# Kernel optimization log

Measured on AMD Instinct MI355X. Metric: run time of the kernel, lower is better.

## Reference

```python
import jax, jax.numpy as jnp
import numpy as np

MASK_RATIO = 0.02
N2V_W, WAV_W, TV_W = 1.0, 0.2, 0.01
THRESHOLD = 50.0
LEVELS = 3


def setup_inputs() -> dict:
    key = jax.random.key(0)
    k1, k2, k3 = jax.random.split(key, 3)
    shape = (64, 1, 512, 512)
    pred = jax.random.uniform(k1, shape, dtype=jnp.float32)
    noisy_input = jax.random.uniform(k2, shape, dtype=jnp.float32)
    # N2V random blind-spot mask (torch.rand_like(pred) < mask_ratio)
    mask = jax.random.uniform(k3, shape, dtype=jnp.float32) < MASK_RATIO
    return {"pred": pred, "noisy_input": noisy_input, "mask": mask}


def haar_dwt2(x):
    # x: [B, H, W] with H, W even. Single-level 2D Haar DWT (pywt 'haar').
    a = x[:, 0::2, 0::2]
    b = x[:, 0::2, 1::2]
    c = x[:, 1::2, 0::2]
    d = x[:, 1::2, 1::2]
    ll = (a + b + c + d) * 0.5
    ch = (a + b - c - d) * 0.5  # horizontal detail
    cv = (a - b + c - d) * 0.5  # vertical detail
    cd = (a - b - c + d) * 0.5  # diagonal detail
    return ll, ch, cv, cd


def _level_l1(c, thr):
    # L1 between coeff and its (detached) soft-thresholded version
    target = jax.lax.stop_gradient(jnp.sign(c) * jnp.maximum(jnp.abs(c) - thr, 0.0))
    return jnp.mean(jnp.abs(c - target))


def reference(pred, noisy_input, mask):
    p = jnp.clip(pred, 0.0, 1.0)

    # --- Noise2Void masked L1 ---
    m = mask.astype(p.dtype)
    n2v = jnp.sum(jnp.abs(p - noisy_input) * m) / jnp.maximum(jnp.sum(m), 1.0)

    # --- Wavelet sparsity (multi-level Haar, soft-threshold targets) ---
    x = p[:, 0]  # [B, H, W]
    details = []  # finest first
    for _ in range(LEVELS):
        x, ch, cv, cd = haar_dwt2(x)
        details.append((ch, cv, cd))
    wav = jnp.asarray(0.0, dtype=p.dtype)
    for level_idx in range(1, LEVELS + 1):  # level_idx=1 -> coarsest (wavedec2 order)
        ch, cv, cd = details[LEVELS - level_idx]
        thr = (THRESHOLD / (2.0 ** (level_idx - 1))) / 255.0
        lvl = (_level_l1(ch, thr) + _level_l1(cv, thr) + _level_l1(cd, thr)) / 3.0
        wav = wav + (1.0 / level_idx) * lvl

    # --- Total variation ---
    tv = jnp.mean(jnp.abs(p[:, :, 1:, :] - p[:, :, :-1, :])) + \
         jnp.mean(jnp.abs(p[:, :, :, 1:] - p[:, :, :, :-1]))

    return N2V_W * n2v + WAV_W * wav + TV_W * tv
```

## Files before the change

### kernel.cpp

```cpp
#include <hip/hip_runtime.h>

#define NIMG 64
#define H 512
#define W 512

constexpr float THR_64  = 50.0f / 255.0f;
constexpr float THR_128 = 50.0f / 2.0f / 255.0f;
constexpr float THR_256 = 50.0f / 4.0f / 255.0f;

__device__ __forceinline__ float wave_sum(float v) {
#pragma unroll
    for (int o = 32; o > 0; o >>= 1) v += __shfl_down(v, o, 64);
    return v;
}

__device__ __forceinline__ float clip01(float x) {
    return fminf(fmaxf(x, 0.0f), 1.0f);
}

__device__ __forceinline__ float4 clip4(float4 p) {
    p.x = clip01(p.x); p.y = clip01(p.y); p.z = clip01(p.z); p.w = clip01(p.w);
    return p;
}

__global__ __launch_bounds__(256, 4) void kA(const float* __restrict__ pred,
                                             const float* __restrict__ noisy,
                                             const int* __restrict__ mask,
                                             float4* __restrict__ pA,
                                             float* __restrict__ pW2,
                                             float* __restrict__ ll2) {
    __shared__ float red[4][5];

    const int tid = threadIdx.x;
    const int lane = tid & 63;
    const int wv = tid >> 6;
    const int w = (blockIdx.x << 2) + wv;
    const int n = w >> 8;
    const int rem = w & 255;
    const int q = rem >> 1;
    const int h = rem & 1;
    const int r0 = q << 2;
    const int col = (h << 8) + (lane << 2);
    const size_t base = (size_t)n * (H * W) + (size_t)r0 * W + col;
    const bool has_halo = (q > 0);
    const size_t baseH = has_halo ? (base - W) : base;

    float4 p0 = *reinterpret_cast<const float4*>(pred + base);
    float4 p1 = *reinterpret_cast<const float4*>(pred + base + W);
    float4 p2 = *reinterpret_cast<const float4*>(pred + base + 2 * W);
    float4 p3 = *reinterpret_cast<const float4*>(pred + base + 3 * W);
    float4 hl = *reinterpret_cast<const float4*>(pred + baseH);
    float4 nz0 = *reinterpret_cast<const float4*>(noisy + base);
    float4 nz1 = *reinterpret_cast<const float4*>(noisy + base + W);
    float4 nz2 = *reinterpret_cast<const float4*>(noisy + base + 2 * W);
    float4 nz3 = *reinterpret_cast<const float4*>(noisy + base + 3 * W);
    int4 mk0 = *reinterpret_cast<const int4*>(mask + base);
    int4 mk1 = *reinterpret_cast<const int4*>(mask + base + W);
    int4 mk2 = *reinterpret_cast<const int4*>(mask + base + 2 * W);
    int4 mk3 = *reinterpret_cast<const int4*>(mask + base + 3 * W);
    float e0 = 0.f, e1 = 0.f, e2 = 0.f, e3 = 0.f;
    const bool edge = (h == 0) && (lane == 63);
    if (edge) {
        e0 = clip01(pred[base + 4]);
        e1 = clip01(pred[base + W + 4]);
        e2 = clip01(pred[base + 2 * W + 4]);
        e3 = clip01(pred[base + 3 * W + 4]);
    }

    p0 = clip4(p0); p1 = clip4(p1); p2 = clip4(p2); p3 = clip4(p3);
    hl = clip4(hl);

    float n2v = 0.0f, msum = 0.0f;
    {
        float m;
        m = mk0.x ? 1.f : 0.f; n2v += fabsf(p0.x - nz0.x) * m; msum += m;
        m = mk0.y ? 1.f : 0.f; n2v += fabsf(p0.y - nz0.y) * m; msum += m;
        m = mk0.z ? 1.f : 0.f; n2v += fabsf(p0.z - nz0.z) * m; msum += m;
        m = mk0.w ? 1.f : 0.f; n2v += fabsf(p0.w - nz0.w) * m; msum += m;
        m = mk1.x ? 1.f : 0.f; n2v += fabsf(p1.x - nz1.x) * m; msum += m;
        m = mk1.y ? 1.f : 0.f; n2v += fabsf(p1.y - nz1.y) * m; msum += m;
        m = mk1.z ? 1.f : 0.f; n2v += fabsf(p1.z - nz1.z) * m; msum += m;
        m = mk1.w ? 1.f : 0.f; n2v += fabsf(p1.w - nz1.w) * m; msum += m;
        m = mk2.x ? 1.f : 0.f; n2v += fabsf(p2.x - nz2.x) * m; msum += m;
        m = mk2.y ? 1.f : 0.f; n2v += fabsf(p2.y - nz2.y) * m; msum += m;
        m = mk2.z ? 1.f : 0.f; n2v += fabsf(p2.z - nz2.z) * m; msum += m;
        m = mk2.w ? 1.f : 0.f; n2v += fabsf(p2.w - nz2.w) * m; msum += m;
        m = mk3.x ? 1.f : 0.f; n2v += fabsf(p3.x - nz3.x) * m; msum += m;
        m = mk3.y ? 1.f : 0.f; n2v += fabsf(p3.y - nz3.y) * m; msum += m;
        m = mk3.z ? 1.f : 0.f; n2v += fabsf(p3.z - nz3.z) * m; msum += m;
        m = mk3.w ? 1.f : 0.f; n2v += fabsf(p3.w - nz3.w) * m; msum += m;
    }

    float tv = 0.0f;
    tv += fabsf(p0.y - p0.x) + fabsf(p0.z - p0.y) + fabsf(p0.w - p0.z);
    tv += fabsf(p1.y - p1.x) + fabsf(p1.z - p1.y) + fabsf(p1.w - p1.z);
    tv += fabsf(p2.y - p2.x) + fabsf(p2.z - p2.y) + fabsf(p2.w - p2.z);
    tv += fabsf(p3.y - p3.x) + fabsf(p3.z - p3.y) + fabsf(p3.w - p3.z);
    float nx0 = __shfl_down(p0.x, 1, 64);
    float nx1 = __shfl_down(p1.x, 1, 64);
    float nx2 = __shfl_down(p2.x, 1, 64);
    float nx3 = __shfl_down(p3.x, 1, 64);
    if (lane < 63) {
        tv += fabsf(nx0 - p0.w) + fabsf(nx1 - p1.w)
            + fabsf(nx2 - p2.w) + fabsf(nx3 - p3.w);
    }
    if (edge) {
        tv += fabsf(e0 - p0.w) + fabsf(e1 - p1.w)
            + fabsf(e2 - p2.w) + fabsf(e3 - p3.w);
    }
    tv += fabsf(p1.x - p0.x) + fabsf(p1.y - p0.y) + fabsf(p1.z - p0.z) + fabsf(p1.w - p0.w);
    tv += fabsf(p2.x - p1.x) + fabsf(p2.y - p1.y) + fabsf(p2.z - p1.z) + fabsf(p2.w - p1.w);
    tv += fabsf(p3.x - p2.x) + fabsf(p3.y - p2.y) + fabsf(p3.z - p2.z) + fabsf(p3.w - p2.w);
    if (has_halo) {
        tv += fabsf(p0.x - hl.x) + fabsf(p0.y - hl.y)
            + fabsf(p0.z - hl.z) + fabsf(p0.w - hl.w);
    }

    float wav1 = 0.0f;
    float llA0, llA1, llB0, llB1;
    {
        float a, b, c, d, ch, cv, cd;
        a = p0.x; b = p0.y; c = p1.x; d = p1.y;
        llA0 = (a + b + c + d) * 0.5f;
        ch = (a + b - c - d) * 0.5f; cv = (a - b + c - d) * 0.5f; cd = (a - b - c + d) * 0.5f;
        wav1 += fminf(fabsf(ch), THR_256) + fminf(fabsf(cv), THR_256) + fminf(fabsf(cd), THR_256);
        a = p0.z; b = p0.w; c = p1.z; d = p1.w;
        llA1 = (a + b + c + d) * 0.5f;
        ch = (a + b - c - d) * 0.5f; cv = (a - b + c - d) * 0.5f; cd = (a - b - c + d) * 0.5f;
        wav1 += fminf(fabsf(ch), THR_256) + fminf(fabsf(cv), THR_256) + fminf(fabsf(cd), THR_256);
        a = p2.x; b = p2.y; c = p3.x; d = p3.y;
        llB0 = (a + b + c + d) * 0.5f;
        ch = (a + b - c - d) * 0.5f; cv = (a - b + c - d) * 0.5f; cd = (a - b - c + d) * 0.5f;
        wav1 += fminf(fabsf(ch), THR_256) + fminf(fabsf(cv), THR_256) + fminf(fabsf(cd), THR_256);
        a = p2.z; b = p2.w; c = p3.z; d = p3.w;
        llB1 = (a + b + c + d) * 0.5f;
        ch = (a + b - c - d) * 0.5f; cv = (a - b + c - d) * 0.5f; cd = (a - b - c + d) * 0.5f;
        wav1 += fminf(fabsf(ch), THR_256) + fminf(fabsf(cv), THR_256) + fminf(fabsf(cd), THR_256);
    }

    float wav2;
    {
        float a = llA0, b = llA1, c = llB0, d = llB1;
        float ll2v = (a + b + c + d) * 0.5f;
        float ch = (a + b - c - d) * 0.5f;
        float cv = (a - b + c - d) * 0.5f;
        float cd = (a - b - c + d) * 0.5f;
        wav2 = fminf(fabsf(ch), THR_128) + fminf(fabsf(cv), THR_128) + fminf(fabsf(cd), THR_128);
        ll2[(size_t)n * 16384 + (size_t)q * 128 + (h << 6) + lane] = ll2v;
    }

    float v0 = wave_sum(n2v);
    float v1 = wave_sum(msum);
    float v2 = wave_sum(tv);
    float v3 = wave_sum(wav1);
    float v4 = wave_sum(wav2);
    if (lane == 0) {
        red[wv][0] = v0; red[wv][1] = v1; red[wv][2] = v2;
        red[wv][3] = v3; red[wv][4] = v4;
    }
    __syncthreads();
    if (tid == 0) {
        pA[blockIdx.x] = make_float4(red[0][0] + red[1][0] + red[2][0] + red[3][0],
                                     red[0][1] + red[1][1] + red[2][1] + red[3][1],
                                     red[0][2] + red[1][2] + red[2][2] + red[3][2],
                                     red[0][3] + red[1][3] + red[2][3] + red[3][3]);
        pW2[blockIdx.x] = red[0][4] + red[1][4] + red[2][4] + red[3][4];
    }
}

__global__ __launch_bounds__(256) void kC(const float* __restrict__ ll2,
                                          float* __restrict__ pC) {
    __shared__ float red[4];
    const int tid = threadIdx.x;
    const int lane = tid & 63, wv = tid >> 6;
    const int bid = blockIdx.x;
    const int n = bid >> 1;
    const int s = bid & 1;
    const float* src = ll2 + (size_t)n * 16384;

    float wav3 = 0.0f;
#pragma unroll
    for (int i = 0; i < 8; ++i) {
        int u = (i << 8) + tid;
        int qr = (s << 5) + (u >> 6);
        int qc = u & 63;
        float2 top = *reinterpret_cast<const float2*>(src + (2 * qr) * 128 + 2 * qc);
        float2 bot = *reinterpret_cast<const float2*>(src + (2 * qr + 1) * 128 + 2 * qc);
        float a = top.x, b = top.y, c = bot.x, d = bot.y;
        float ch = (a + b - c - d) * 0.5f;
        float cv = (a - b + c - d) * 0.5f;
        float cd = (a - b - c + d) * 0.5f;
        wav3 += fminf(fabsf(ch), THR_64) + fminf(fabsf(cv), THR_64) + fminf(fabsf(cd), THR_64);
    }
    float v = wave_sum(wav3);
    if (lane == 0) red[wv] = v;
    __syncthreads();
    if (tid == 0) pC[bid] = red[0] + red[1] + red[2] + red[3];
}

__global__ __launch_bounds__(256) void kD(const float4* __restrict__ pA,
                                          const float* __restrict__ pW2,
                                          const float* __restrict__ pC,
                                          float* __restrict__ out) {
    __shared__ float red[4][6];
    const int tid = threadIdx.x;
    const int lane = tid & 63, wv = tid >> 6;

    float s0 = 0, s1 = 0, s2 = 0, s3 = 0, s4 = 0, s5 = 0;
#pragma unroll
    for (int j = 0; j < 16; ++j) {
        float4 v = pA[tid + (j << 8)];
        s0 += v.x; s1 += v.y; s2 += v.z; s3 += v.w;
        s4 += pW2[tid + (j << 8)];
    }
    if (tid < 128) s5 = pC[tid];

    s0 = wave_sum(s0); s1 = wave_sum(s1); s2 = wave_sum(s2);
    s3 = wave_sum(s3); s4 = wave_sum(s4); s5 = wave_sum(s5);
    if (lane == 0) {
        red[wv][0] = s0; red[wv][1] = s1; red[wv][2] = s2;
        red[wv][3] = s3; red[wv][4] = s4; red[wv][5] = s5;
    }
    __syncthreads();
    if (tid == 0) {
        float a0 = red[0][0] + red[1][0] + red[2][0] + red[3][0];
        float a1 = red[0][1] + red[1][1] + red[2][1] + red[3][1];
        float a2 = red[0][2] + red[1][2] + red[2][2] + red[3][2];
        float a3 = red[0][3] + red[1][3] + red[2][3] + red[3][3];
        float a4 = red[0][4] + red[1][4] + red[2][4] + red[3][4];
        float a5 = red[0][5] + red[1][5] + red[2][5] + red[3][5];
        float n2v = a0 / fmaxf(a1, 1.0f);
        float tv = a2 / 16744448.0f;
        float wav = a3 * (1.0f / 37748736.0f)
                  + a4 * (1.0f / 6291456.0f)
                  + a5 * (1.0f / 786432.0f);
        out[0] = 1.0f * n2v + 0.2f * wav + 0.01f * tv;
    }
}

extern "C" void kernel_launch(void* const* d_in, const int* in_sizes, int n_in,
                              void* d_out, int out_size, void* d_ws, size_t ws_size,
                              hipStream_t stream) {
    (void)in_sizes; (void)n_in; (void)out_size; (void)ws_size;
    const float* pred  = (const float*)d_in[0];
    const float* noisy = (const float*)d_in[1];
    const int*   mask  = (const int*)d_in[2];

    float4* pA  = (float4*)d_ws;
    float*  pW2 = (float*)((char*)d_ws + 65536);
    float*  pC  = (float*)((char*)d_ws + 81920);
    float*  ll2 = (float*)((char*)d_ws + 98304);

    kA<<<4096, 256, 0, stream>>>(pred, noisy, mask, pA, pW2, ll2);
    kC<<<128, 256, 0, stream>>>(ll2, pC);
    kD<<<1, 256, 0, stream>>>(pA, pW2, pC, (float*)d_out);
}
```

Before: 197.5 us.

## Stage 8-row pred tiles in LDS with one halo row per block

Each block now loads a contiguous 8-row by 512-column tile of pred, noisy and mask with fully coalesced float4 loads, clips pred once and writes it to shared memory, plus a single halo row. The per-wave TV and Haar computations then read from LDS, so the redundant halo-row and edge-column global loads are replaced by shared reads. It adds a __syncthreads and 18 KB of LDS per block, and drops the occupancy hint from launch bounds. The grid mapping changes from 4 waves of independent 4-row strips to 64 blocks per image.

```diff
diff --git a/kernel.cpp b/kernel.cpp
--- a/kernel.cpp
+++ b/kernel.cpp
@@ -23,73 +23,61 @@
     return p;
 }
 
-__global__ __launch_bounds__(256, 4) void kA(const float* __restrict__ pred,
-                                             const float* __restrict__ noisy,
-                                             const int* __restrict__ mask,
-                                             float4* __restrict__ pA,
-                                             float* __restrict__ pW2,
-                                             float* __restrict__ ll2) {
+__global__ __launch_bounds__(256) void kA(const float* __restrict__ pred,
+                                          const float* __restrict__ noisy,
+                                          const int* __restrict__ mask,
+                                          float4* __restrict__ pA,
+                                          float* __restrict__ pW2,
+                                          float* __restrict__ ll2) {
+    __shared__ float sl[9 * 512];
     __shared__ float red[4][5];
 
     const int tid = threadIdx.x;
     const int lane = tid & 63;
     const int wv = tid >> 6;
-    const int w = (blockIdx.x << 2) + wv;
-    const int n = w >> 8;
-    const int rem = w & 255;
-    const int q = rem >> 1;
-    const int h = rem & 1;
-    const int r0 = q << 2;
-    const int col = (h << 8) + (lane << 2);
-    const size_t base = (size_t)n * (H * W) + (size_t)r0 * W + col;
-    const bool has_halo = (q > 0);
-    const size_t baseH = has_halo ? (base - W) : base;
-
-    float4 p0 = *reinterpret_cast<const float4*>(pred + base);
-    float4 p1 = *reinterpret_cast<const float4*>(pred + base + W);
-    float4 p2 = *reinterpret_cast<const float4*>(pred + base + 2 * W);
-    float4 p3 = *reinterpret_cast<const float4*>(pred + base + 3 * W);
-    float4 hl = *reinterpret_cast<const float4*>(pred + baseH);
-    float4 nz0 = *reinterpret_cast<const float4*>(noisy + base);
-    float4 nz1 = *reinterpret_cast<const float4*>(noisy + base + W);
-    float4 nz2 = *reinterpret_cast<const float4*>(noisy + base + 2 * W);
-    float4 nz3 = *reinterpret_cast<const float4*>(noisy + base + 3 * W);
-    int4 mk0 = *reinterpret_cast<const int4*>(mask + base);
-    int4 mk1 = *reinterpret_cast<const int4*>(mask + base + W);
-    int4 mk2 = *reinterpret_cast<const int4*>(mask + base + 2 * W);
-    int4 mk3 = *reinterpret_cast<const int4*>(mask + base + 3 * W);
-    float e0 = 0.f, e1 = 0.f, e2 = 0.f, e3 = 0.f;
-    const bool edge = (h == 0) && (lane == 63);
-    if (edge) {
-        e0 = clip01(pred[base + 4]);
-        e1 = clip01(pred[base + W + 4]);
-        e2 = clip01(pred[base + 2 * W + 4]);
-        e3 = clip01(pred[base + 3 * W + 4]);
-    }
-
-    p0 = clip4(p0); p1 = clip4(p1); p2 = clip4(p2); p3 = clip4(p3);
-    hl = clip4(hl);
+    const int bid = blockIdx.x;
+    const int n = bid >> 6;
+    const int s = bid & 63;
+    const int r0 = s << 3;
+    const size_t base = (size_t)n * (H * W) + (size_t)r0 * W;
 
     float n2v = 0.0f, msum = 0.0f;
-    {
+#pragma unroll
+    for (int k = 0; k < 4; ++k) {
+        const int idx = tid + (k << 8);
+        const size_t off = base + (size_t)idx * 4;
+        float4 p = *reinterpret_cast<const float4*>(pred + off);
+        float4 nz = *reinterpret_cast<const float4*>(noisy + off);
+        int4 mk = *reinterpret_cast<const int4*>(mask + off);
+        p = clip4(p);
         float m;
-        m = mk0.x ? 1.f : 0.f; n2v += fabsf(p0.x - nz0.x) * m; msum += m;
-        m = mk0.y ? 1.f : 0.f; n2v += fabsf(p0.y - nz0.y) * m; msum += m;
-        m = mk0.z ? 1.f : 0.f; n2v += fabsf(p0.z - nz0.z) * m; msum += m;
-        m = mk0.w ? 1.f : 0.f; n2v += fabsf(p0.w - nz0.w) * m; msum += m;
-        m = mk1.x ? 1.f : 0.f; n2v += fabsf(p1.x - nz1.x) * m; msum += m;
-        m = mk1.y ? 1.f : 0.f; n2v += fabsf(p1.y - nz1.y) * m; msum += m;
-        m = mk1.z ? 1.f : 0.f; n2v += fabsf(p1.z - nz1.z) * m; msum += m;
-        m = mk1.w ? 1.f : 0.f; n2v += fabsf(p1.w - nz1.w) * m; msum += m;
-        m = mk2.x ? 1.f : 0.f; n2v += fabsf(p2.x - nz2.x) * m; msum += m;
-        m = mk2.y ? 1.f : 0.f; n2v += fabsf(p2.y - nz2.y) * m; msum += m;
-        m = mk2.z ? 1.f : 0.f; n2v += fabsf(p2.z - nz2.z) * m; msum += m;
-        m = mk2.w ? 1.f : 0.f; n2v += fabsf(p2.w - nz2.w) * m; msum += m;
-        m = mk3.x ? 1.f : 0.f; n2v += fabsf(p3.x - nz3.x) * m; msum += m;
-        m = mk3.y ? 1.f : 0.f; n2v += fabsf(p3.y - nz3.y) * m; msum += m;
-        m = mk3.z ? 1.f : 0.f; n2v += fabsf(p3.z - nz3.z) * m; msum += m;
-        m = mk3.w ? 1.f : 0.f; n2v += fabsf(p3.w - nz3.w) * m; msum += m;
-    }
+        m = mk.x ? 1.f : 0.f; n2v += fabsf(p.x - nz.x) * m; msum += m;
+        m = mk.y ? 1.f : 0.f; n2v += fabsf(p.y - nz.y) * m; msum += m;
+        m = mk.z ? 1.f : 0.f; n2v += fabsf(p.z - nz.z) * m; msum += m;
+        m = mk.w ? 1.f : 0.f; n2v += fabsf(p.w - nz.w) * m; msum += m;
+        *reinterpret_cast<float4*>(&sl[idx << 2]) = p;
+    }
+    if (tid < 128) {
+        float4 hp = make_float4(0.f, 0.f, 0.f, 0.f);
+        if (r0 > 0) {
+            hp = clip4(*reinterpret_cast<const float4*>(pred + base - W + (size_t)tid * 4));
+        }
+        *reinterpret_cast<float4*>(&sl[(8 << 9) + (tid << 2)]) = hp;
+    }
+    __syncthreads();
+
+    const int q2 = wv >> 1;
+    const int h = wv & 1;
+    const int cofs = (h << 8) + (lane << 2);
+    const float* rowp = sl + (q2 << 11);
+
+    float4 p0 = *reinterpret_cast<const float4*>(rowp + cofs);
+    float4 p1 = *reinterpret_cast<const float4*>(rowp + 512 + cofs);
+    float4 p2 = *reinterpret_cast<const float4*>(rowp + 1024 + cofs);
+    float4 p3 = *reinterpret_cast<const float4*>(rowp + 1536 + cofs);
+    const float* hrow = (q2 == 1) ? (sl + 3 * 512) : (sl + 8 * 512);
+    float4 hl = *reinterpret_cast<const float4*>(hrow + cofs);
+    const bool has_halo = (q2 == 1) || (r0 > 0);
 
     float tv = 0.0f;
     tv += fabsf(p0.y - p0.x) + fabsf(p0.z - p0.y) + fabsf(p0.w - p0.z);
@@ -103,10 +91,9 @@
     if (lane < 63) {
         tv += fabsf(nx0 - p0.w) + fabsf(nx1 - p1.w)
             + fabsf(nx2 - p2.w) + fabsf(nx3 - p3.w);
-    }
-    if (edge) {
-        tv += fabsf(e0 - p0.w) + fabsf(e1 - p1.w)
-            + fabsf(e2 - p2.w) + fabsf(e3 - p3.w);
+    } else if (h == 0) {
+        tv += fabsf(rowp[256] - p0.w) + fabsf(rowp[512 + 256] - p1.w)
+            + fabsf(rowp[1024 + 256] - p2.w) + fabsf(rowp[1536 + 256] - p3.w);
     }
     tv += fabsf(p1.x - p0.x) + fabsf(p1.y - p0.y) + fabsf(p1.z - p0.z) + fabsf(p1.w - p0.w);
     tv += fabsf(p2.x - p1.x) + fabsf(p2.y - p1.y) + fabsf(p2.z - p1.z) + fabsf(p2.w - p1.w);
@@ -117,37 +104,35 @@
     }
 
     float wav1 = 0.0f;
-    float llA0, llA1, llB0, llB1;
+    float a, b, c, d, ch, cv, cd;
+    a = p0.x; b = p0.y; c = p1.x; d = p1.y;
+    float llA0 = (a + b + c + d) * 0.5f;
+    ch = (a + b - c - d) * 0.5f; cv = (a - b + c - d) * 0.5f; cd = (a - b - c + d) * 0.5f;
+    wav1 += fminf(fabsf(ch), THR_256) + fminf(fabsf(cv), THR_256) + fminf(fabsf(cd), THR_256);
+    a = p0.z; b = p0.w; c = p1.z; d = p1.w;
+    float llA1 = (a + b + c + d) * 0.5f;
+    ch = (a + b - c - d) * 0.5f; cv = (a - b + c - d) * 0.5f; cd = (a - b - c + d) * 0.5f;
+    wav1 += fminf(fabsf(ch), THR_256) + fminf(fabsf(cv), THR_256) + fminf(fabsf(cd), THR_256);
+    a = p2.x; b = p2.y; c = p3.x; d = p3.y;
+    float llB0 = (a + b + c + d) * 0.5f;
+    ch = (a + b - c - d) * 0.5f; cv = (a - b + c - d) * 0.5f; cd = (a - b - c + d) * 0.5f;
+    wav1 += fminf(fabsf(ch), THR_256) + fminf(fabsf(cv), THR_256) + fminf(fabsf(cd), THR_256);
+    a = p2.z; b = p2.w; c = p3.z; d = p3.w;
+    float llB1 = (a + b + c + d) * 0.5f;
+    ch = (a + b - c - d) * 0.5f; cv = (a - b + c - d) * 0.5f; cd = (a - b - c + d) * 0.5f;
+    wav1 += fminf(fabsf(ch), THR_256) + fminf(fabsf(cv), THR_256) + fminf(fabsf(cd), THR_256);
+
+    float wav2;
+    float ll2v;
     {
-        float a, b, c, d, ch, cv, cd;
-        a = p0.x; b = p0.y; c = p1.x; d = p1.y;
-        llA0 = (a + b + c + d) * 0.5f;
-        ch = (a + b - c - d) * 0.5f; cv = (a - b + c - d) * 0.5f; cd = (a - b - c + d) * 0.5f;
-        wav1 += fminf(fabsf(ch), THR_256) + fminf(fabsf(cv), THR_256) + fminf(fabsf(cd), THR_256);
-        a = p0.z; b = p0.w; c = p1.z; d = p1.w;
-        llA1 = (a + b + c + d) * 0.5f;
-        ch = (a + b - c - d) * 0.5f; cv = (a - b + c - d) * 0.5f; cd = (a - b - c + d) * 0.5f;
-        wav1 += fminf(fabsf(ch), THR_256) + fminf(fabsf(cv), THR_256) + fminf(fabsf(cd), THR_256);
-        a = p2.x; b = p2.y; c = p3.x; d = p3.y;
-        llB0 = (a + b + c + d) * 0.5f;
-        ch = (a + b - c - d) * 0.5f; cv = (a - b + c - d) * 0.5f; cd = (a - b - c + d) * 0.5f;
-        wav1 += fminf(fabsf(ch), THR_256) + fminf(fabsf(cv), THR_256) + fminf(fabsf(cd), THR_256);
-        a = p2.z; b = p2.w; c = p3.z; d = p3.w;
-        llB1 = (a + b + c + d) * 0.5f;
-        ch = (a + b - c - d) * 0.5f; cv = (a - b + c - d) * 0.5f; cd = (a - b - c + d) * 0.5f;
-        wav1 += fminf(fabsf(ch), THR_256) + fminf(fabsf(cv), THR_256) + fminf(fabsf(cd), THR_256);
-    }
-
-    float wav2;
-    {
-        float a = llA0, b = llA1, c = llB0, d = llB1;
-        float ll2v = (a + b + c + d) * 0.5f;
-        float ch = (a + b - c - d) * 0.5f;
-        float cv = (a - b + c - d) * 0.5f;
-        float cd = (a - b - c + d) * 0.5f;
+        a = llA0; b = llA1; c = llB0; d = llB1;
+        ll2v = (a + b + c + d) * 0.5f;
+        ch = (a + b - c - d) * 0.5f;
+        cv = (a - b + c - d) * 0.5f;
+        cd = (a - b - c + d) * 0.5f;
         wav2 = fminf(fabsf(ch), THR_128) + fminf(fabsf(cv), THR_128) + fminf(fabsf(cd), THR_128);
-        ll2[(size_t)n * 16384 + (size_t)q * 128 + (h << 6) + lane] = ll2v;
-    }
+    }
+    ll2[(size_t)n * 16384 + (size_t)((s << 1) + q2) * 128 + (h << 6) + lane] = ll2v;
 
     float v0 = wave_sum(n2v);
     float v1 = wave_sum(msum);
@@ -160,11 +145,11 @@
     }
     __syncthreads();
     if (tid == 0) {
-        pA[blockIdx.x] = make_float4(red[0][0] + red[1][0] + red[2][0] + red[3][0],
-                                     red[0][1] + red[1][1] + red[2][1] + red[3][1],
-                                     red[0][2] + red[1][2] + red[2][2] + red[3][2],
-                                     red[0][3] + red[1][3] + red[2][3] + red[3][3]);
-        pW2[blockIdx.x] = red[0][4] + red[1][4] + red[2][4] + red[3][4];
+        pA[bid] = make_float4(red[0][0] + red[1][0] + red[2][0] + red[3][0],
+                              red[0][1] + red[1][1] + red[2][1] + red[3][1],
+                              red[0][2] + red[1][2] + red[2][2] + red[3][2],
+                              red[0][3] + red[1][3] + red[2][3] + red[3][3]);
+        pW2[bid] = red[0][4] + red[1][4] + red[2][4] + red[3][4];
     }
 }
 
```

Measured after the change: 198.7 us. Within noise of the previous version (+0.6%).
